# Optimization experiments

Measured on AMD Instinct MI355X. Metric: run time of the kernel, lower is better.

## Reference

```python
import jax, jax.numpy as jnp
import numpy as np

DIM = 1024
HEADS = 16
DH = DIM // HEADS  # 64
DFF = 4096
EPS = 1e-5


def layer_norm(x, g, b):
    mu = jnp.mean(x, axis=-1, keepdims=True)
    var = jnp.mean(jnp.square(x - mu), axis=-1, keepdims=True)
    return (x - mu) * jax.lax.rsqrt(var + EPS) * g + b


def setup_inputs() -> dict:
    key = jax.random.key(0)
    ks = jax.random.split(key, 12)
    s = 0.02
    return {
        "encoder_input": jax.random.normal(ks[0], (4, 2048, DIM), jnp.float32),
        # per-head Q/K/V projections stacked over heads: [H, dim, d_head]
        "wq": jax.random.normal(ks[1], (HEADS, DIM, DH), jnp.float32) * s,
        "bq": jnp.zeros((HEADS, DH), jnp.float32),
        "wk": jax.random.normal(ks[2], (HEADS, DIM, DH), jnp.float32) * s,
        "bk": jnp.zeros((HEADS, DH), jnp.float32),
        "wv": jax.random.normal(ks[3], (HEADS, DIM, DH), jnp.float32) * s,
        "bv": jnp.zeros((HEADS, DH), jnp.float32),
        "ln1_g": jnp.ones((DIM,), jnp.float32),
        "ln1_b": jnp.zeros((DIM,), jnp.float32),
        "w1": jax.random.normal(ks[4], (DIM, DFF), jnp.float32) * s,
        "b1": jnp.zeros((DFF,), jnp.float32),
        "w2": jax.random.normal(ks[5], (DFF, DIM), jnp.float32) * s,
        "b2": jnp.zeros((DIM,), jnp.float32),
        "ln2_g": jnp.ones((DIM,), jnp.float32),
        "ln2_b": jnp.zeros((DIM,), jnp.float32),
    }


def reference(encoder_input, wq, bq, wk, bk, wv, bv, ln1_g, ln1_b,
              w1, b1, w2, b2, ln2_g, ln2_b):
    x = encoder_input  # [B, S, D]
    B, S, D = x.shape
    # per-head projections, batched over heads (same math as the head loop)
    q = jnp.einsum('bsd,hde->bhse', x, wq) + bq[None, :, None, :]
    k = jnp.einsum('bsd,hde->bhse', x, wk) + bk[None, :, None, :]
    v = jnp.einsum('bsd,hde->bhse', x, wv) + bv[None, :, None, :]
    scores = jnp.einsum('bhse,bhte->bhst', q, k) / jnp.sqrt(jnp.float32(DH))
    attn = jax.nn.softmax(scores, axis=-1)
    o = jnp.einsum('bhst,bhte->bhse', attn, v)  # [B, H, S, dh]
    self_attn = jnp.transpose(o, (0, 2, 1, 3)).reshape(B, S, D)  # concat heads on dim=2
    # residual: source + LayerNorm(target)  (dropout = identity in eval)
    res1 = x + layer_norm(self_attn, ln1_g, ln1_b)
    ff = jax.nn.relu(res1 @ w1 + b1) @ w2 + b2
    return res1 + layer_norm(ff, ln2_g, ln2_b)
```

## Files before the change

### kernel.cpp

```cpp
#include <hip/hip_runtime.h>
#include <cstdint>
#include <cmath>

typedef unsigned short u16;
using bf16x8 = __attribute__((ext_vector_type(8))) __bf16;
using f32x4  = __attribute__((ext_vector_type(4))) float;

#define MFMA(a, b, c) __builtin_amdgcn_mfma_f32_16x16x32_bf16((a), (b), (c), 0, 0, 0)

__device__ __forceinline__ float b2f(u16 u) {
    union { unsigned int i; float f; } x; x.i = ((unsigned int)u) << 16; return x.f;
}
__device__ __forceinline__ u16 f2b(float f) {
    union { float f; unsigned int i; } x; x.f = f;
    unsigned int r = x.i + 0x7FFFu + ((x.i >> 16) & 1u);
    return (u16)(r >> 16);
}
__device__ __forceinline__ u16 cvtb(float f) {
    __bf16 h = (__bf16)f;
    return *reinterpret_cast<u16*>(&h);
}
__device__ __forceinline__ uint32_t cvtpk(float lo, float hi) {
    uint32_t r;
    asm("v_cvt_pk_bf16_f32 %0, %1, %2" : "=v"(r) : "v"(lo), "v"(hi));
    return r;
}

__device__ __forceinline__ void gload16(const u16* g, u16* l) {
    __builtin_amdgcn_global_load_lds(
        (const __attribute__((address_space(1))) void*)g,
        (__attribute__((address_space(3))) void*)l, 16, 0, 0);
}

#define BAR do { asm volatile("" ::: "memory"); \
                 __builtin_amdgcn_s_barrier();  \
                 asm volatile("" ::: "memory"); } while (0)

__global__ __launch_bounds__(256) void xcvt_kernel(const float* __restrict__ X,
                                                   u16* __restrict__ Xb)
{
    size_t i = ((size_t)blockIdx.x * 256 + threadIdx.x) * 8;
    float4 a = *reinterpret_cast<const float4*>(&X[i]);
    float4 b = *reinterpret_cast<const float4*>(&X[i + 4]);
    ushort4 lo = {f2b(a.x), f2b(a.y), f2b(a.z), f2b(a.w)};
    ushort4 hi = {f2b(b.x), f2b(b.y), f2b(b.z), f2b(b.w)};
    *reinterpret_cast<ushort4*>(&Xb[i]) = lo;
    *reinterpret_cast<ushort4*>(&Xb[i + 4]) = hi;
}

__global__ __launch_bounds__(256) void wT_kernel(const float* __restrict__ W,
                                                 u16* __restrict__ Wt, int K, int N)
{
    __shared__ __align__(16) u16 Ts[64][72];
    const int k0 = blockIdx.x * 64, n0 = blockIdx.y * 64;
    const int tid = threadIdx.x;
    #pragma unroll
    for (int it = 0; it < 4; ++it) {
        int vI = tid + it * 256;
        int kr = vI >> 4, nc = (vI & 15) * 4;
        float4 f = *reinterpret_cast<const float4*>(&W[(size_t)(k0 + kr) * N + n0 + nc]);
        Ts[nc + 0][kr] = f2b(f.x);
        Ts[nc + 1][kr] = f2b(f.y);
        Ts[nc + 2][kr] = f2b(f.z);
        Ts[nc + 3][kr] = f2b(f.w);
    }
    __syncthreads();
    #pragma unroll
    for (int it = 0; it < 2; ++it) {
        int vI = tid + it * 256;
        int nr = vI >> 3, kc = (vI & 7) * 8;
        *reinterpret_cast<uint4*>(&Wt[(size_t)(n0 + nr) * K + k0 + kc]) =
            *reinterpret_cast<uint4*>(&Ts[nr][kc]);
    }
}

__global__ __launch_bounds__(256) void wqkvT_kernel(
    const float* __restrict__ Wq, const float* __restrict__ Wk,
    const float* __restrict__ Wv, u16* __restrict__ Wt)
{
    __shared__ __align__(16) u16 Ts[64][72];
    const int k0 = blockIdx.x * 64, h = blockIdx.y, m = blockIdx.z;
    const float* W = (m == 0 ? Wq : (m == 1 ? Wk : Wv)) + (size_t)h * 65536;
    const int tid = threadIdx.x;
    #pragma unroll
    for (int it = 0; it < 4; ++it) {
        int vI = tid + it * 256;
        int kr = vI >> 4, dc = (vI & 15) * 4;
        float4 f = *reinterpret_cast<const float4*>(&W[(size_t)(k0 + kr) * 64 + dc]);
        Ts[dc + 0][kr] = f2b(f.x);
        Ts[dc + 1][kr] = f2b(f.y);
        Ts[dc + 2][kr] = f2b(f.z);
        Ts[dc + 3][kr] = f2b(f.w);
    }
    __syncthreads();
    #pragma unroll
    for (int it = 0; it < 2; ++it) {
        int vI = tid + it * 256;
        int dr = vI >> 3, kc = (vI & 7) * 8;
        *reinterpret_cast<uint4*>(
            &Wt[((size_t)(m * 1024 + h * 64 + dr)) * 1024 + k0 + kc]) =
            *reinterpret_cast<uint4*>(&Ts[dr][kc]);
    }
}

__global__ __launch_bounds__(256) void biascat_kernel(
    const float* __restrict__ Bq, const float* __restrict__ Bk,
    const float* __restrict__ Bv, float* __restrict__ out)
{
    int i = blockIdx.x * 256 + threadIdx.x;
    const float* B = (i < 1024 ? Bq : (i < 2048 ? Bk : Bv));
    out[i] = B[i & 1023];
}

__device__ __forceinline__ void stage_half(const u16* __restrict__ gb, int K,
                                           u16* lr, int lane, int w)
{
    #pragma unroll
    for (int cc = 0; cc < 2; ++cc) {
        int c = w * 2 + cc;
        int l = c * 64 + lane;
        int lp = l ^ ((l >> 3) & 7);
        gload16(gb + (size_t)(lp >> 3) * K + (lp & 7) * 8, lr + c * 512);
    }
}

template <int RELU, int F32OUT>
__global__ __launch_bounds__(512, 2) void gemm8(
    const u16* __restrict__ A, const u16* __restrict__ Bt,
    const float* __restrict__ bias, void* __restrict__ Cv,
    int M, int N, int K)
{
    __shared__ __align__(16) u16 lds[65536];
    const int tid = threadIdx.x, lane = tid & 63, w = tid >> 6;
    const int wm = w >> 2, wn = w & 3;
    const int g = lane >> 4, ln = lane & 15;
    const int xr = (ln & 7) << 3;
    const int brow = (wn & 1) * 64;

    int nwg = gridDim.x * gridDim.y;
    int bid = blockIdx.y * gridDim.x + blockIdx.x;
    int swz = (bid & 7) * (nwg >> 3) + (bid >> 3);
    const int m0 = (swz % gridDim.x) * 256;
    const int n0 = (swz / gridDim.x) * 256;

    const u16* Ab = A + (size_t)m0 * K;
    const u16* Bb = Bt + (size_t)n0 * K;

    u16* ldsA[2] = { lds + wm * 8192,         lds + 32768 + wm * 8192 };
    u16* ldsB[2] = { lds + 16384 + (wn >> 1) * 8192,
                     lds + 49152 + (wn >> 1) * 8192 };

    f32x4 acc[8][4];
    #pragma unroll
    for (int i = 0; i < 8; ++i)
        #pragma unroll
        for (int j = 0; j < 4; ++j) acc[i][j] = (f32x4){0.f, 0.f, 0.f, 0.f};

    bf16x8 af[4][2], bf[2][2];

#define RD_A(d, mh)                                                           \
    _Pragma("unroll") for (int i = 0; i < 4; ++i)                             \
    _Pragma("unroll") for (int kk = 0; kk < 2; ++kk)                          \
        af[i][kk] = *(const bf16x8*)&ldsA[d][((mh)*64 + i*16 + ln)*64 +       \
                                             ((kk*32 + g*8) ^ xr)];
#define RD_B(d, nh)                                                           \
    _Pragma("unroll") for (int j = 0; j < 2; ++j)                             \
    _Pragma("unroll") for (int kk = 0; kk < 2; ++kk)                          \
        bf[j][kk] = *(const bf16x8*)&ldsB[d][(brow + (nh)*32 + j*16 + ln)*64  \
                                             + ((kk*32 + g*8) ^ xr)];
#define MMQ(mh, nh)                                                           \
    __builtin_amdgcn_s_setprio(1);                                            \
    _Pragma("unroll") for (int i = 0; i < 4; ++i)                             \
    _Pragma("unroll") for (int j = 0; j < 2; ++j) {                           \
        acc[(mh)*4+i][(nh)*2+j] =                                             \
            MFMA(af[i][0], bf[j][0], acc[(mh)*4+i][(nh)*2+j]);                \
        acc[(mh)*4+i][(nh)*2+j] =                                             \
            MFMA(af[i][1], bf[j][1], acc[(mh)*4+i][(nh)*2+j]);                \
    }                                                                         \
    __builtin_amdgcn_s_setprio(0);

    const int ntk = K >> 6;
    const int nit = ntk >> 1;

    stage_half(Ab,                           K, lds + 0,     lane, w);
    stage_half(Ab + (size_t)128 * K,         K, lds + 8192,  lane, w);
    stage_half(Bb,                           K, lds + 16384, lane, w);
    stage_half(Bb + (size_t)128 * K,         K, lds + 24576, lane, w);
    stage_half(Ab + 64,                      K, lds + 32768, lane, w);
    stage_half(Ab + (size_t)128 * K + 64,    K, lds + 40960, lane, w);
    asm volatile("s_waitcnt vmcnt(4)" ::: "memory");
    BAR;

    for (int u = 0; u < nit; ++u) {
        const int t1 = 2 * u + 1;
        int s0 = 2 * u + 2; if (s0 >= ntk) s0 = ntk - 1;
        int s1 = 2 * u + 3; if (s1 >= ntk) s1 = ntk - 1;
        RD_A(0, 0); RD_B(0, 0);
        stage_half(Bb + (size_t)t1 * 64, K, lds + 49152, lane, w);
        BAR; MMQ(0, 0); BAR;
        RD_B(0, 1);
        stage_half(Bb + (size_t)128 * K + (size_t)t1 * 64, K, lds + 57344, lane, w);
        BAR; MMQ(0, 1); BAR;
        RD_A(0, 1); RD_B(0, 0);
        BAR; MMQ(1, 0); BAR;
        RD_B(0, 1);
        stage_half(Ab + (size_t)s0 * 64, K, lds + 0, lane, w);
        BAR; MMQ(1, 1);
        asm volatile("s_waitcnt vmcnt(2)" ::: "memory");
        BAR;
        RD_A(1, 0); RD_B(1, 0);
        stage_half(Ab + (size_t)128 * K + (size_t)s0 * 64, K, lds + 8192, lane, w);
        BAR; MMQ(0, 0); BAR;
        RD_B(1, 1);
        stage_half(Bb + (size_t)s0 * 64, K, lds + 16384, lane, w);
        BAR; MMQ(0, 1); BAR;
        RD_A(1, 1); RD_B(1, 0);
        stage_half(Bb + (size_t)128 * K + (size_t)s0 * 64, K, lds + 24576, lane, w);
        BAR; MMQ(1, 0); BAR;
        RD_B(1, 1);
        stage_half(Ab + (size_t)s1 * 64, K, lds + 32768, lane, w);
        stage_half(Ab + (size_t)128 * K + (size_t)s1 * 64, K, lds + 40960, lane, w);
        BAR; MMQ(1, 1);
        asm volatile("s_waitcnt vmcnt(4)" ::: "memory");
        BAR;
    }
#undef RD_A
#undef RD_B
#undef MMQ

    asm volatile("s_waitcnt vmcnt(0)" ::: "memory");
    BAR;

    if (F32OUT) {
        float* C = (float*)Cv;
        float bv[4];
        #pragma unroll
        for (int j = 0; j < 4; ++j) bv[j] = bias[n0 + wn * 64 + j * 16 + ln];
        #pragma unroll
        for (int i = 0; i < 8; ++i)
            #pragma unroll
            for (int j = 0; j < 4; ++j)
                #pragma unroll
                for (int r = 0; r < 4; ++r) {
                    float v = acc[i][j][r] + bv[j];
                    if (RELU) v = fmaxf(v, 0.f);
                    int row = m0 + wm * 128 + i * 16 + g * 4 + r;
                    int col = n0 + wn * 64 + j * 16 + ln;
                    C[(size_t)row * N + col] = v;
                }
    } else {
        u16* C = (u16*)Cv;
        float bv[4];
        #pragma unroll
        for (int j = 0; j < 4; ++j) bv[j] = bias[n0 + wn * 64 + j * 16 + ln];
        #pragma unroll
        for (int i = 0; i < 8; ++i)
            #pragma unroll
            for (int j = 0; j < 4; ++j)
                #pragma unroll
                for (int r = 0; r < 4; ++r) {
                    float v = acc[i][j][r] + bv[j];
                    if (RELU) v = fmaxf(v, 0.f);
                    int row = wm * 128 + i * 16 + g * 4 + r;
                    int col = wn * 64 + j * 16 + ln;
                    lds[row * 256 + (col ^ ((row & 12) << 2))] = cvtb(v);
                }
        BAR;
        #pragma unroll
        for (int p = 0; p < 16; ++p) {
            int f = (p * 512 + tid) * 8;
            int row = f >> 8, col = f & 255;
            uint4 val = *(uint4*)&lds[row * 256 + (col ^ ((row & 12) << 2))];
            *(uint4*)&C[(size_t)(m0 + row) * N + n0 + col] = val;
        }
    }
}

template <int RELU, int F32OUT>
__global__ __launch_bounds__(512, 2) void gemm3(
    const u16* __restrict__ A, const u16* __restrict__ Bt,
    const float* __restrict__ bias, void* __restrict__ Cv,
    int M, int N, int K)
{
    __shared__ __align__(16) u16 lds[73728];
    const int tid = threadIdx.x, lane = tid & 63, w = tid >> 6;
    const int wm = w >> 2, wn = w & 3;
    const int g = lane >> 4, ln = lane & 15;
    const int xr = (ln & 7) << 3;
    const int bro = (wn & 1) * 64;

    int nwg = gridDim.x * gridDim.y;
    int bid = blockIdx.y * gridDim.x + blockIdx.x;
    int swz = (bid & 7) * (nwg >> 3) + (bid >> 3);
    const int m0 = (swz % gridDim.x) * 128;
    const int n0 = (swz / gridDim.x) * 256;

    const u16* Ab = A + (size_t)m0 * K;
    const u16* Bb = Bt + (size_t)n0 * K;

    f32x4 acc[4][4];
    #pragma unroll
    for (int i = 0; i < 4; ++i)
        #pragma unroll
        for (int j = 0; j < 4; ++j) acc[i][j] = (f32x4){0.f, 0.f, 0.f, 0.f};

    const int ntk = K >> 6;

    #pragma unroll
    for (int u = 0; u < 2; ++u) {
        stage_half(Ab + (size_t)u * 64, K, lds + u * 24576, lane, w);
        stage_half(Bb + (size_t)u * 64, K, lds + u * 24576 + 8192, lane, w);
        stage_half(Bb + (size_t)128 * K + (size_t)u * 64, K,
                   lds + u * 24576 + 16384, lane, w);
    }

    bf16x8 af[4][2], bf[2][2];

    for (int u = 0; u < ntk; ++u) {
        const int p = u % 3;
        if (u < ntk - 1) asm volatile("s_waitcnt vmcnt(6)" ::: "memory");
        else             asm volatile("s_waitcnt vmcnt(0)" ::: "memory");
        BAR;
        u16* bufA = lds + p * 24576;
        u16* bufB = lds + p * 24576 + 8192 + (wn >> 1) * 8192;
        const int us = u + 2;
        const int ps = us % 3;
        #pragma unroll
        for (int i = 0; i < 4; ++i)
            #pragma unroll
            for (int kk = 0; kk < 2; ++kk)
                af[i][kk] = *(const bf16x8*)&bufA[(wm * 64 + i * 16 + ln) * 64 +
                                                 ((kk * 32 + g * 8) ^ xr)];
        #pragma unroll
        for (int j = 0; j < 2; ++j)
            #pragma unroll
            for (int kk = 0; kk < 2; ++kk)
                bf[j][kk] = *(const bf16x8*)&bufB[(bro + j * 16 + ln) * 64 +
                                                  ((kk * 32 + g * 8) ^ xr)];
        if (us < ntk)
            stage_half(Ab + (size_t)us * 64, K, lds + ps * 24576, lane, w);
        __builtin_amdgcn_s_setprio(1);
        #pragma unroll
        for (int i = 0; i < 4; ++i)
            #pragma unroll
            for (int j = 0; j < 2; ++j) {
                acc[i][j] = MFMA(af[i][0], bf[j][0], acc[i][j]);
                acc[i][j] = MFMA(af[i][1], bf[j][1], acc[i][j]);
            }
        __builtin_amdgcn_s_setprio(0);
        #pragma unroll
        for (int j = 0; j < 2; ++j)
            #pragma unroll
            for (int kk = 0; kk < 2; ++kk)
                bf[j][kk] = *(const bf16x8*)&bufB[(bro + 32 + j * 16 + ln) * 64 +
                                                  ((kk * 32 + g * 8) ^ xr)];
        if (us < ntk) {
            stage_half(Bb + (size_t)us * 64, K, lds + ps * 24576 + 8192, lane, w);
            stage_half(Bb + (size_t)128 * K + (size_t)us * 64, K,
                       lds + ps * 24576 + 16384, lane, w);
        }
        __builtin_amdgcn_s_setprio(1);
        #pragma unroll
        for (int i = 0; i < 4; ++i)
            #pragma unroll
            for (int j = 0; j < 2; ++j) {
                acc[i][2 + j] = MFMA(af[i][0], bf[j][0], acc[i][2 + j]);
                acc[i][2 + j] = MFMA(af[i][1], bf[j][1], acc[i][2 + j]);
            }
        __builtin_amdgcn_s_setprio(0);
    }

    float bv[4];
    #pragma unroll
    for (int j = 0; j < 4; ++j) bv[j] = bias[n0 + wn * 64 + j * 16 + ln];

    if (F32OUT) {
        float* C = (float*)Cv;
        #pragma unroll
        for (int i = 0; i < 4; ++i)
            #pragma unroll
            for (int j = 0; j < 4; ++j)
                #pragma unroll
                for (int r = 0; r < 4; ++r) {
                    float v = acc[i][j][r] + bv[j];
                    if (RELU) v = fmaxf(v, 0.f);
                    int row = m0 + wm * 64 + i * 16 + g * 4 + r;
                    int col = n0 + wn * 64 + j * 16 + ln;
                    C[(size_t)row * N + col] = v;
                }
    } else {
        u16* C = (u16*)Cv;
        BAR;
        #pragma unroll
        for (int i = 0; i < 4; ++i)
            #pragma unroll
            for (int j = 0; j < 4; ++j)
                #pragma unroll
                for (int r = 0; r < 4; ++r) {
                    float v = acc[i][j][r] + bv[j];
                    if (RELU) v = fmaxf(v, 0.f);
                    int row = wm * 64 + i * 16 + g * 4 + r;
                    int col = wn * 64 + j * 16 + ln;
                    lds[row * 256 + (col ^ ((row & 12) << 2))] = cvtb(v);
                }
        BAR;
        #pragma unroll
        for (int p2 = 0; p2 < 8; ++p2) {
            int f = (p2 * 512 + tid) * 8;
            int row = f >> 8, col = f & 255;
            uint4 val = *(uint4*)&lds[row * 256 + (col ^ ((row & 12) << 2))];
            *(uint4*)&C[(size_t)(m0 + row) * N + n0 + col] = val;
        }
    }
}

__device__ __forceinline__ int sperm(int row) {
    return (row & 32) | ((row & 12) << 1) | ((row & 16) >> 2) | (row & 3);
}

__global__ __launch_bounds__(256, 2) void attn_kernel(
    const u16* __restrict__ QKV, u16* __restrict__ O)
{
    const int bh = blockIdx.x, b = bh >> 4, h = bh & 15;
    const int q0 = blockIdx.y * 256;
    const int tid = threadIdx.x;
    const int lane = tid & 63, w = tid >> 6;
    const int g = lane >> 4, ln = lane & 15;

    __shared__ __align__(16) u16 Ks[2][64][72];
    __shared__ __align__(16) u16 Vt2[2][64][72];

    const u16* Qp = QKV + (size_t)b * 2048 * 3072 + h * 64;
    const u16* Kp = Qp + 1024;
    const u16* Vp = Qp + 2048;

    bf16x8 qf[2][2][2];
    #pragma unroll
    for (int G = 0; G < 2; ++G)
        #pragma unroll
        for (int i = 0; i < 2; ++i)
            #pragma unroll
            for (int kk = 0; kk < 2; ++kk)
                qf[G][i][kk] = *reinterpret_cast<const bf16x8*>(
                    &Qp[(size_t)(q0 + G * 128 + w * 32 + i * 16 + ln) * 3072 +
                        kk * 32 + g * 8]);

    f32x4 oacc[2][2][4];
    #pragma unroll
    for (int G = 0; G < 2; ++G)
        #pragma unroll
        for (int i = 0; i < 2; ++i)
            #pragma unroll
            for (int n = 0; n < 4; ++n) oacc[G][i][n] = (f32x4){0.f, 0.f, 0.f, 0.f};
    float mrun[2][2] = {{-1e30f, -1e30f}, {-1e30f, -1e30f}};
    float lsum[2][2] = {{0.f, 0.f}, {0.f, 0.f}};

    const float C1 = 0.125f * 1.44269504f;

    const int r0 = tid >> 3, c0 = (tid & 7) * 8;
    const int r1 = r0 + 32;
    const int ss0 = sperm(r0) ^ c0;
    const int ss1 = sperm(r1) ^ c0;

    {
        uint4 ka = *reinterpret_cast<const uint4*>(&Kp[(size_t)r0 * 3072 + c0]);
        uint4 kb = *reinterpret_cast<const uint4*>(&Kp[(size_t)r1 * 3072 + c0]);
        uint4 va = *reinterpret_cast<const uint4*>(&Vp[(size_t)r0 * 3072 + c0]);
        uint4 vb = *reinterpret_cast<const uint4*>(&Vp[(size_t)r1 * 3072 + c0]);
        *reinterpret_cast<uint4*>(&Ks[0][r0][c0]) = ka;
        *reinterpret_cast<uint4*>(&Ks[0][r1][c0]) = kb;
        const u16* tva = reinterpret_cast<const u16*>(&va);
        const u16* tvb = reinterpret_cast<const u16*>(&vb);
        #pragma unroll
        for (int j = 0; j < 8; ++j) {
            Vt2[0][c0 + j][ss0] = tva[j];
            Vt2[0][c0 + j][ss1] = tvb[j];
        }
    }
    __syncthreads();

    for (int t = 0; t < 32; ++t) {
        const int c = t & 1;
        uint4 ka, kb, va, vb;
        if (t < 31) {
            const size_t rb0 = (size_t)((t + 1) * 64 + r0) * 3072 + c0;
            const size_t rb1 = (size_t)((t + 1) * 64 + r1) * 3072 + c0;
            ka = *reinterpret_cast<const uint4*>(&Kp[rb0]);
            kb = *reinterpret_cast<const uint4*>(&Kp[rb1]);
            va = *reinterpret_cast<const uint4*>(&Vp[rb0]);
            vb = *reinterpret_cast<const uint4*>(&Vp[rb1]);
        }

        uint32_t pk[2][2][8];
        #pragma unroll
        for (int G = 0; G < 2; ++G) {
            f32x4 sc[4][2];
            #pragma unroll
            for (int j = 0; j < 4; ++j)
                #pragma unroll
                for (int i = 0; i < 2; ++i) sc[j][i] = (f32x4){0.f, 0.f, 0.f, 0.f};
            #pragma unroll
            for (int kk = 0; kk < 2; ++kk)
                #pragma unroll
                for (int j = 0; j < 4; ++j) {
                    bf16x8 kf = *(const bf16x8*)&Ks[c][j * 16 + ln][kk * 32 + g * 8];
                    sc[j][0] = MFMA(kf, qf[G][0][kk], sc[j][0]);
                    sc[j][1] = MFMA(kf, qf[G][1][kk], sc[j][1]);
                }

            float tl[2];
            #pragma unroll
            for (int i = 0; i < 2; ++i) {
                float t01 = fmaxf(fmaxf(sc[0][i][0], sc[0][i][1]),
                                  fmaxf(sc[0][i][2], sc[0][i][3]));
                float t23 = fmaxf(fmaxf(sc[1][i][0], sc[1][i][1]),
                                  fmaxf(sc[1][i][2], sc[1][i][3]));
                float t45 = fmaxf(fmaxf(sc[2][i][0], sc[2][i][1]),
                                  fmaxf(sc[2][i][2], sc[2][i][3]));
                float t67 = fmaxf(fmaxf(sc[3][i][0], sc[3][i][1]),
                                  fmaxf(sc[3][i][2], sc[3][i][3]));
                tl[i] = fmaxf(fmaxf(t01, t23), fmaxf(t45, t67)) * C1;
            }
            int small_ = (tl[0] <= mrun[G][0] + 10.f) && (tl[1] <= mrun[G][1] + 10.f);
            if (!__all(small_)) {
                #pragma unroll
                for (int i = 0; i < 2; ++i) {
                    float tt = tl[i];
                    tt = fmaxf(tt, __shfl_xor(tt, 16));
                    tt = fmaxf(tt, __shfl_xor(tt, 32));
                    float mn = fmaxf(mrun[G][i], tt);
                    float al = exp2f(mrun[G][i] - mn);
                    mrun[G][i] = mn;
                    lsum[G][i] *= al;
                    #pragma unroll
                    for (int r = 0; r < 4; ++r) {
                        float alr = __shfl(al, g * 4 + r);
                        #pragma unroll
                        for (int n = 0; n < 4; ++n) oacc[G][i][n][r] *= alr;
                    }
                }
            }
            #pragma unroll
            for (int i = 0; i < 2; ++i) {
                float m_ = mrun[G][i];
                float ps = 0.f;
                #pragma unroll
                for (int j = 0; j < 4; ++j) {
                    #pragma unroll
                    for (int r = 0; r < 4; ++r) {
                        float p = exp2f(fmaf(sc[j][i][r], C1, -m_));
                        sc[j][i][r] = p;
                        ps += p;
                    }
                    pk[G][i][j * 2 + 0] = cvtpk(sc[j][i][0], sc[j][i][1]);
                    pk[G][i][j * 2 + 1] = cvtpk(sc[j][i][2], sc[j][i][3]);
                }
                lsum[G][i] += ps;
            }
        }

        #pragma unroll
        for (int kk = 0; kk < 2; ++kk) {
            union { uint32_t u[4]; bf16x8 v; } a[2][2];
            #pragma unroll
            for (int G = 0; G < 2; ++G)
                #pragma unroll
                for (int i = 0; i < 2; ++i) {
                    a[G][i].u[0] = pk[G][i][kk * 4 + 0];
                    a[G][i].u[1] = pk[G][i][kk * 4 + 1];
                    a[G][i].u[2] = pk[G][i][kk * 4 + 2];
                    a[G][i].u[3] = pk[G][i][kk * 4 + 3];
                }
            #pragma unroll
            for (int n = 0; n < 4; ++n) {
                int d = n * 16 + ln;
                bf16x8 vf = *(const bf16x8*)&Vt2[c][d][(kk * 32 + g * 8) ^ (d & 56)];
                oacc[0][0][n] = MFMA(a[0][0].v, vf, oacc[0][0][n]);
                oacc[0][1][n] = MFMA(a[0][1].v, vf, oacc[0][1][n]);
                oacc[1][0][n] = MFMA(a[1][0].v, vf, oacc[1][0][n]);
                oacc[1][1][n] = MFMA(a[1][1].v, vf, oacc[1][1][n]);
            }
        }

        if (t < 31) {
            *reinterpret_cast<uint4*>(&Ks[c ^ 1][r0][c0]) = ka;
            *reinterpret_cast<uint4*>(&Ks[c ^ 1][r1][c0]) = kb;
            const u16* tva = reinterpret_cast<const u16*>(&va);
            const u16* tvb = reinterpret_cast<const u16*>(&vb);
            #pragma unroll
            for (int j = 0; j < 8; ++j) {
                Vt2[c ^ 1][c0 + j][ss0] = tva[j];
                Vt2[c ^ 1][c0 + j][ss1] = tvb[j];
            }
        }
        __syncthreads();
    }

    #pragma unroll
    for (int G = 0; G < 2; ++G)
        #pragma unroll
        for (int i = 0; i < 2; ++i) {
            float s = lsum[G][i];
            s += __shfl_xor(s, 16);
            s += __shfl_xor(s, 32);
            float rinv = __builtin_amdgcn_rcpf(s);
            #pragma unroll
            for (int r = 0; r < 4; ++r) {
                float rv = __shfl(rinv, g * 4 + r);
                int row = q0 + G * 128 + w * 32 + i * 16 + g * 4 + r;
                #pragma unroll
                for (int n = 0; n < 4; ++n)
                    O[((size_t)(b * 2048 + row)) * 1024 + h * 64 + n * 16 + ln] =
                        cvtb(oacc[G][i][n][r] * rv);
            }
        }
}

template <int T_F32, int SRC_F32, int OUT_F32>
__global__ __launch_bounds__(256) void ln_add_kernel(
    const void* __restrict__ TV, const void* __restrict__ SrcV,
    const float* __restrict__ G, const float* __restrict__ Bt,
    void* __restrict__ OutV)
{
    const int row = blockIdx.x;
    const int tid = threadIdx.x;
    __shared__ float red[8];

    const size_t rb = (size_t)row * 1024;
    float v0, v1, v2, v3;
    if (T_F32) {
        float4 tv = *reinterpret_cast<const float4*>((const float*)TV + rb + tid * 4);
        v0 = tv.x; v1 = tv.y; v2 = tv.z; v3 = tv.w;
    } else {
        ushort4 tv = *reinterpret_cast<const ushort4*>((const u16*)TV + rb + tid * 4);
        v0 = b2f(tv.x); v1 = b2f(tv.y); v2 = b2f(tv.z); v3 = b2f(tv.w);
    }
    float s = v0 + v1 + v2 + v3;
    float sq = v0 * v0 + v1 * v1 + v2 * v2 + v3 * v3;
    #pragma unroll
    for (int mm = 1; mm < 64; mm <<= 1) {
        s += __shfl_xor(s, mm);
        sq += __shfl_xor(sq, mm);
    }
    if ((tid & 63) == 0) { red[tid >> 6] = s; red[4 + (tid >> 6)] = sq; }
    __syncthreads();
    s = red[0] + red[1] + red[2] + red[3];
    sq = red[4] + red[5] + red[6] + red[7];
    float mu = s * (1.f / 1024.f);
    float var = sq * (1.f / 1024.f) - mu * mu;
    float rs = rsqrtf(var + 1e-5f);

    float s0, s1, s2, s3;
    if (SRC_F32) {
        float4 sv = *reinterpret_cast<const float4*>((const float*)SrcV + rb + tid * 4);
        s0 = sv.x; s1 = sv.y; s2 = sv.z; s3 = sv.w;
    } else {
        ushort4 sv = *reinterpret_cast<const ushort4*>((const u16*)SrcV + rb + tid * 4);
        s0 = b2f(sv.x); s1 = b2f(sv.y); s2 = b2f(sv.z); s3 = b2f(sv.w);
    }
    float4 gv = *reinterpret_cast<const float4*>(&G[tid * 4]);
    float4 bv = *reinterpret_cast<const float4*>(&Bt[tid * 4]);
    float o0 = s0 + (v0 - mu) * rs * gv.x + bv.x;
    float o1 = s1 + (v1 - mu) * rs * gv.y + bv.y;
    float o2 = s2 + (v2 - mu) * rs * gv.z + bv.z;
    float o3 = s3 + (v3 - mu) * rs * gv.w + bv.w;
    if (OUT_F32) {
        float4 ov = {o0, o1, o2, o3};
        *reinterpret_cast<float4*>((float*)OutV + rb + tid * 4) = ov;
    } else {
        ushort4 ov = {f2b(o0), f2b(o1), f2b(o2), f2b(o3)};
        *reinterpret_cast<ushort4*>((u16*)OutV + rb + tid * 4) = ov;
    }
}

extern "C" void kernel_launch(void* const* d_in, const int* in_sizes, int n_in,
                              void* d_out, int out_size, void* d_ws, size_t ws_size,
                              hipStream_t stream)
{
    const float* X   = (const float*)d_in[0];
    const float* Wq  = (const float*)d_in[1];
    const float* Bq  = (const float*)d_in[2];
    const float* Wk  = (const float*)d_in[3];
    const float* Bk  = (const float*)d_in[4];
    const float* Wv  = (const float*)d_in[5];
    const float* Bv  = (const float*)d_in[6];
    const float* g1  = (const float*)d_in[7];
    const float* b1  = (const float*)d_in[8];
    const float* W1  = (const float*)d_in[9];
    const float* B1  = (const float*)d_in[10];
    const float* W2  = (const float*)d_in[11];
    const float* B2  = (const float*)d_in[12];
    const float* g2  = (const float*)d_in[13];
    const float* b2  = (const float*)d_in[14];
    float* out = (float*)d_out;

    char* ws = (char*)d_ws;
    const size_t MiB = 1048576;
    u16*   qkv   = (u16*)(ws);
    u16*   Xb    = (u16*)(ws + 48 * MiB);
    u16*   attnb = (u16*)(ws + 48 * MiB);
    u16*   wqkvt = (u16*)(ws + 64 * MiB);
    float* bcat  = (float*)(ws + 70 * MiB);
    u16*   res1  = (u16*)(ws + 64 * MiB);
    u16*   hid   = (u16*)(ws);
    u16*   w1t   = (u16*)(ws + 80 * MiB);
    u16*   w2t   = (u16*)(ws + 88 * MiB);

    xcvt_kernel<<<4096, 256, 0, stream>>>(X, Xb);
    wT_kernel<<<dim3(16, 64), 256, 0, stream>>>(W1, w1t, 1024, 4096);
    wT_kernel<<<dim3(64, 16), 256, 0, stream>>>(W2, w2t, 4096, 1024);
    wqkvT_kernel<<<dim3(16, 16, 3), 256, 0, stream>>>(Wq, Wk, Wv, wqkvt);
    biascat_kernel<<<12, 256, 0, stream>>>(Bq, Bk, Bv, bcat);

    gemm3<0, 0><<<dim3(64, 12), 512, 0, stream>>>(Xb, wqkvt, bcat, qkv, 8192, 3072, 1024);
    attn_kernel<<<dim3(64, 8), 256, 0, stream>>>(qkv, attnb);
    ln_add_kernel<0, 1, 0><<<8192, 256, 0, stream>>>(attnb, X, g1, b1, res1);

    gemm8<1, 0><<<dim3(32, 16), 512, 0, stream>>>(res1, w1t, B1, hid, 8192, 4096, 1024);
    gemm3<0, 1><<<dim3(64, 4), 512, 0, stream>>>(hid, w2t, B2, out, 8192, 1024, 4096);
    ln_add_kernel<1, 0, 1><<<8192, 256, 0, stream>>>(out, res1, g2, b2, out);
}
```

Before: 364.6 us.

## Split attention block across 8 waves, one 32-row query group each

The attention kernel moves from 256 threads with each wave handling two 32-row query groups to 512 threads with each wave handling one group. K/V tile loading is spread across twice as many threads, so each thread loads one row instead of two. The aim is to cut per-thread register pressure and raise wave-level parallelism and latency hiding (launch bounds 512,4). The cost is more waves contending at each barrier and less reuse of each K/V LDS fragment read per wave.

```diff
diff --git a/kernel.cpp b/kernel.cpp
--- a/kernel.cpp
+++ b/kernel.cpp
@@ -418,7 +418,7 @@
     return (row & 32) | ((row & 12) << 1) | ((row & 16) >> 2) | (row & 3);
 }
 
-__global__ __launch_bounds__(256, 2) void attn_kernel(
+__global__ __launch_bounds__(512, 4) void attn_kernel(
     const u16* __restrict__ QKV, u16* __restrict__ O)
 {
     const int bh = blockIdx.x, b = bh >> 4, h = bh & 15;
@@ -434,186 +434,152 @@
     const u16* Kp = Qp + 1024;
     const u16* Vp = Qp + 2048;
 
-    bf16x8 qf[2][2][2];
-    #pragma unroll
-    for (int G = 0; G < 2; ++G)
-        #pragma unroll
-        for (int i = 0; i < 2; ++i)
-            #pragma unroll
-            for (int kk = 0; kk < 2; ++kk)
-                qf[G][i][kk] = *reinterpret_cast<const bf16x8*>(
-                    &Qp[(size_t)(q0 + G * 128 + w * 32 + i * 16 + ln) * 3072 +
-                        kk * 32 + g * 8]);
-
-    f32x4 oacc[2][2][4];
-    #pragma unroll
-    for (int G = 0; G < 2; ++G)
-        #pragma unroll
-        for (int i = 0; i < 2; ++i)
-            #pragma unroll
-            for (int n = 0; n < 4; ++n) oacc[G][i][n] = (f32x4){0.f, 0.f, 0.f, 0.f};
-    float mrun[2][2] = {{-1e30f, -1e30f}, {-1e30f, -1e30f}};
-    float lsum[2][2] = {{0.f, 0.f}, {0.f, 0.f}};
+    bf16x8 qf[2][2];
+    #pragma unroll
+    for (int i = 0; i < 2; ++i)
+        #pragma unroll
+        for (int kk = 0; kk < 2; ++kk)
+            qf[i][kk] = *reinterpret_cast<const bf16x8*>(
+                &Qp[(size_t)(q0 + w * 32 + i * 16 + ln) * 3072 + kk * 32 + g * 8]);
+
+    f32x4 oacc[2][4];
+    #pragma unroll
+    for (int i = 0; i < 2; ++i)
+        #pragma unroll
+        for (int n = 0; n < 4; ++n) oacc[i][n] = (f32x4){0.f, 0.f, 0.f, 0.f};
+    float mrun[2] = {-1e30f, -1e30f};
+    float lsum[2] = {0.f, 0.f};
 
     const float C1 = 0.125f * 1.44269504f;
 
     const int r0 = tid >> 3, c0 = (tid & 7) * 8;
-    const int r1 = r0 + 32;
     const int ss0 = sperm(r0) ^ c0;
-    const int ss1 = sperm(r1) ^ c0;
 
     {
         uint4 ka = *reinterpret_cast<const uint4*>(&Kp[(size_t)r0 * 3072 + c0]);
-        uint4 kb = *reinterpret_cast<const uint4*>(&Kp[(size_t)r1 * 3072 + c0]);
         uint4 va = *reinterpret_cast<const uint4*>(&Vp[(size_t)r0 * 3072 + c0]);
-        uint4 vb = *reinterpret_cast<const uint4*>(&Vp[(size_t)r1 * 3072 + c0]);
         *reinterpret_cast<uint4*>(&Ks[0][r0][c0]) = ka;
-        *reinterpret_cast<uint4*>(&Ks[0][r1][c0]) = kb;
         const u16* tva = reinterpret_cast<const u16*>(&va);
-        const u16* tvb = reinterpret_cast<const u16*>(&vb);
-        #pragma unroll
-        for (int j = 0; j < 8; ++j) {
-            Vt2[0][c0 + j][ss0] = tva[j];
-            Vt2[0][c0 + j][ss1] = tvb[j];
-        }
+        #pragma unroll
+        for (int j = 0; j < 8; ++j) Vt2[0][c0 + j][ss0] = tva[j];
     }
     __syncthreads();
 
     for (int t = 0; t < 32; ++t) {
         const int c = t & 1;
-        uint4 ka, kb, va, vb;
+        uint4 ka, va;
         if (t < 31) {
             const size_t rb0 = (size_t)((t + 1) * 64 + r0) * 3072 + c0;
-            const size_t rb1 = (size_t)((t + 1) * 64 + r1) * 3072 + c0;
             ka = *reinterpret_cast<const uint4*>(&Kp[rb0]);
-            kb = *reinterpret_cast<const uint4*>(&Kp[rb1]);
             va = *reinterpret_cast<const uint4*>(&Vp[rb0]);
-            vb = *reinterpret_cast<const uint4*>(&Vp[rb1]);
-        }
-
-        uint32_t pk[2][2][8];
-        #pragma unroll
-        for (int G = 0; G < 2; ++G) {
-            f32x4 sc[4][2];
-            #pragma unroll
-            for (int j = 0; j < 4; ++j)
+        }
+
+        f32x4 sc[4][2];
+        #pragma unroll
+        for (int j = 0; j < 4; ++j)
+            #pragma unroll
+            for (int i = 0; i < 2; ++i) sc[j][i] = (f32x4){0.f, 0.f, 0.f, 0.f};
+        #pragma unroll
+        for (int kk = 0; kk < 2; ++kk)
+            #pragma unroll
+            for (int j = 0; j < 4; ++j) {
+                bf16x8 kf = *(const bf16x8*)&Ks[c][j * 16 + ln][kk * 32 + g * 8];
+                sc[j][0] = MFMA(kf, qf[0][kk], sc[j][0]);
+                sc[j][1] = MFMA(kf, qf[1][kk], sc[j][1]);
+            }
+
+        float tl[2];
+        #pragma unroll
+        for (int i = 0; i < 2; ++i) {
+            float t01 = fmaxf(fmaxf(sc[0][i][0], sc[0][i][1]),
+                              fmaxf(sc[0][i][2], sc[0][i][3]));
+            float t23 = fmaxf(fmaxf(sc[1][i][0], sc[1][i][1]),
+                              fmaxf(sc[1][i][2], sc[1][i][3]));
+            float t45 = fmaxf(fmaxf(sc[2][i][0], sc[2][i][1]),
+                              fmaxf(sc[2][i][2], sc[2][i][3]));
+            float t67 = fmaxf(fmaxf(sc[3][i][0], sc[3][i][1]),
+                              fmaxf(sc[3][i][2], sc[3][i][3]));
+            tl[i] = fmaxf(fmaxf(t01, t23), fmaxf(t45, t67)) * C1;
+        }
+        int small_ = (tl[0] <= mrun[0] + 10.f) && (tl[1] <= mrun[1] + 10.f);
+        if (!__all(small_)) {
+            #pragma unroll
+            for (int i = 0; i < 2; ++i) {
+                float tt = tl[i];
+                tt = fmaxf(tt, __shfl_xor(tt, 16));
+                tt = fmaxf(tt, __shfl_xor(tt, 32));
+                float mn = fmaxf(mrun[i], tt);
+                float al = exp2f(mrun[i] - mn);
+                mrun[i] = mn;
+                lsum[i] *= al;
                 #pragma unroll
-                for (int i = 0; i < 2; ++i) sc[j][i] = (f32x4){0.f, 0.f, 0.f, 0.f};
-            #pragma unroll
-            for (int kk = 0; kk < 2; ++kk)
-                #pragma unroll
-                for (int j = 0; j < 4; ++j) {
-                    bf16x8 kf = *(const bf16x8*)&Ks[c][j * 16 + ln][kk * 32 + g * 8];
-                    sc[j][0] = MFMA(kf, qf[G][0][kk], sc[j][0]);
-                    sc[j][1] = MFMA(kf, qf[G][1][kk], sc[j][1]);
-                }
-
-            float tl[2];
-            #pragma unroll
-            for (int i = 0; i < 2; ++i) {
-                float t01 = fmaxf(fmaxf(sc[0][i][0], sc[0][i][1]),
-                                  fmaxf(sc[0][i][2], sc[0][i][3]));
-                float t23 = fmaxf(fmaxf(sc[1][i][0], sc[1][i][1]),
-                                  fmaxf(sc[1][i][2], sc[1][i][3]));
-                float t45 = fmaxf(fmaxf(sc[2][i][0], sc[2][i][1]),
-                                  fmaxf(sc[2][i][2], sc[2][i][3]));
-                float t67 = fmaxf(fmaxf(sc[3][i][0], sc[3][i][1]),
-                                  fmaxf(sc[3][i][2], sc[3][i][3]));
-                tl[i] = fmaxf(fmaxf(t01, t23), fmaxf(t45, t67)) * C1;
-            }
-            int small_ = (tl[0] <= mrun[G][0] + 10.f) && (tl[1] <= mrun[G][1] + 10.f);
-            if (!__all(small_)) {
-                #pragma unroll
-                for (int i = 0; i < 2; ++i) {
-                    float tt = tl[i];
-                    tt = fmaxf(tt, __shfl_xor(tt, 16));
-                    tt = fmaxf(tt, __shfl_xor(tt, 32));
-                    float mn = fmaxf(mrun[G][i], tt);
-                    float al = exp2f(mrun[G][i] - mn);
-                    mrun[G][i] = mn;
-                    lsum[G][i] *= al;
+                for (int r = 0; r < 4; ++r) {
+                    float alr = __shfl(al, g * 4 + r);
                     #pragma unroll
-                    for (int r = 0; r < 4; ++r) {
-                        float alr = __shfl(al, g * 4 + r);
-                        #pragma unroll
-                        for (int n = 0; n < 4; ++n) oacc[G][i][n][r] *= alr;
-                    }
+                    for (int n = 0; n < 4; ++n) oacc[i][n][r] *= alr;
                 }
             }
-            #pragma unroll
-            for (int i = 0; i < 2; ++i) {
-                float m_ = mrun[G][i];
-                float ps = 0.f;
+        }
+        uint32_t pk[2][8];
+        #pragma unroll
+        for (int i = 0; i < 2; ++i) {
+            float m_ = mrun[i];
+            float ps = 0.f;
+            #pragma unroll
+            for (int j = 0; j < 4; ++j) {
                 #pragma unroll
-                for (int j = 0; j < 4; ++j) {
-                    #pragma unroll
-                    for (int r = 0; r < 4; ++r) {
-                        float p = exp2f(fmaf(sc[j][i][r], C1, -m_));
-                        sc[j][i][r] = p;
-                        ps += p;
-                    }
-                    pk[G][i][j * 2 + 0] = cvtpk(sc[j][i][0], sc[j][i][1]);
-                    pk[G][i][j * 2 + 1] = cvtpk(sc[j][i][2], sc[j][i][3]);
+                for (int r = 0; r < 4; ++r) {
+                    float p = exp2f(fmaf(sc[j][i][r], C1, -m_));
+                    sc[j][i][r] = p;
+                    ps += p;
                 }
-                lsum[G][i] += ps;
+                pk[i][j * 2 + 0] = cvtpk(sc[j][i][0], sc[j][i][1]);
+                pk[i][j * 2 + 1] = cvtpk(sc[j][i][2], sc[j][i][3]);
             }
+            lsum[i] += ps;
         }
 
         #pragma unroll
         for (int kk = 0; kk < 2; ++kk) {
-            union { uint32_t u[4]; bf16x8 v; } a[2][2];
-            #pragma unroll
-            for (int G = 0; G < 2; ++G)
-                #pragma unroll
-                for (int i = 0; i < 2; ++i) {
-                    a[G][i].u[0] = pk[G][i][kk * 4 + 0];
-                    a[G][i].u[1] = pk[G][i][kk * 4 + 1];
-                    a[G][i].u[2] = pk[G][i][kk * 4 + 2];
-                    a[G][i].u[3] = pk[G][i][kk * 4 + 3];
-                }
+            union { uint32_t u[4]; bf16x8 v; } a0, a1;
+            a0.u[0] = pk[0][kk * 4 + 0]; a0.u[1] = pk[0][kk * 4 + 1];
+            a0.u[2] = pk[0][kk * 4 + 2]; a0.u[3] = pk[0][kk * 4 + 3];
+            a1.u[0] = pk[1][kk * 4 + 0]; a1.u[1] = pk[1][kk * 4 + 1];
+            a1.u[2] = pk[1][kk * 4 + 2]; a1.u[3] = pk[1][kk * 4 + 3];
             #pragma unroll
             for (int n = 0; n < 4; ++n) {
                 int d = n * 16 + ln;
                 bf16x8 vf = *(const bf16x8*)&Vt2[c][d][(kk * 32 + g * 8) ^ (d & 56)];
-                oacc[0][0][n] = MFMA(a[0][0].v, vf, oacc[0][0][n]);
-                oacc[0][1][n] = MFMA(a[0][1].v, vf, oacc[0][1][n]);
-                oacc[1][0][n] = MFMA(a[1][0].v, vf, oacc[1][0][n]);
-                oacc[1][1][n] = MFMA(a[1][1].v, vf, oacc[1][1][n]);
+                oacc[0][n] = MFMA(a0.v, vf, oacc[0][n]);
+                oacc[1][n] = MFMA(a1.v, vf, oacc[1][n]);
             }
         }
 
         if (t < 31) {
             *reinterpret_cast<uint4*>(&Ks[c ^ 1][r0][c0]) = ka;
-            *reinterpret_cast<uint4*>(&Ks[c ^ 1][r1][c0]) = kb;
             const u16* tva = reinterpret_cast<const u16*>(&va);
-            const u16* tvb = reinterpret_cast<const u16*>(&vb);
-            #pragma unroll
-            for (int j = 0; j < 8; ++j) {
-                Vt2[c ^ 1][c0 + j][ss0] = tva[j];
-                Vt2[c ^ 1][c0 + j][ss1] = tvb[j];
-            }
+            #pragma unroll
+            for (int j = 0; j < 8; ++j) Vt2[c ^ 1][c0 + j][ss0] = tva[j];
         }
         __syncthreads();
     }
 
     #pragma unroll
-    for (int G = 0; G < 2; ++G)
-        #pragma unroll
-        for (int i = 0; i < 2; ++i) {
-            float s = lsum[G][i];
-            s += __shfl_xor(s, 16);
-            s += __shfl_xor(s, 32);
-            float rinv = __builtin_amdgcn_rcpf(s);
-            #pragma unroll
-            for (int r = 0; r < 4; ++r) {
-                float rv = __shfl(rinv, g * 4 + r);
-                int row = q0 + G * 128 + w * 32 + i * 16 + g * 4 + r;
-                #pragma unroll
-                for (int n = 0; n < 4; ++n)
-                    O[((size_t)(b * 2048 + row)) * 1024 + h * 64 + n * 16 + ln] =
-                        cvtb(oacc[G][i][n][r] * rv);
-            }
-        }
+    for (int i = 0; i < 2; ++i) {
+        float s = lsum[i];
+        s += __shfl_xor(s, 16);
+        s += __shfl_xor(s, 32);
+        float rinv = __builtin_amdgcn_rcpf(s);
+        #pragma unroll
+        for (int r = 0; r < 4; ++r) {
+            float rv = __shfl(rinv, g * 4 + r);
+            int row = q0 + w * 32 + i * 16 + g * 4 + r;
+            #pragma unroll
+            for (int n = 0; n < 4; ++n)
+                O[((size_t)(b * 2048 + row)) * 1024 + h * 64 + n * 16 + ln] =
+                    cvtb(oacc[i][n][r] * rv);
+        }
+    }
 }
 
 template <int T_F32, int SRC_F32, int OUT_F32>
@@ -713,7 +679,7 @@
     biascat_kernel<<<12, 256, 0, stream>>>(Bq, Bk, Bv, bcat);
 
     gemm3<0, 0><<<dim3(64, 12), 512, 0, stream>>>(Xb, wqkvt, bcat, qkv, 8192, 3072, 1024);
-    attn_kernel<<<dim3(64, 8), 256, 0, stream>>>(qkv, attnb);
+    attn_kernel<<<dim3(64, 8), 512, 0, stream>>>(qkv, attnb);
     ln_add_kernel<0, 1, 0><<<8192, 256, 0, stream>>>(attnb, X, g1, b1, res1);
 
     gemm8<1, 0><<<dim3(32, 16), 512, 0, stream>>>(res1, w1t, B1, hid, 8192, 4096, 1024);
```

New measurement: 359.8 us. No clear change (-1.3%).
